# Kernel tuning notes

Hardware: AMD Instinct MI355X
Metric: run time of the kernel (lower is better)

## Reference

```python
import jax, jax.numpy as jnp
import numpy as np

N = 50000          # nodes
E = 800000         # edges (before self-loops)
IN = 128           # in_dim
HID = 128          # hidden_dim
HEADS = 4
G = 256            # graphs in batch
EPS = 1e-5         # batchnorm eps
NEG_SLOPE = 0.2    # GATConv leaky_relu slope


def _gat_layer(x, src, dst, W, a_src, a_dst, bias, H, C, concat):
    """PyG-style GATConv (self-loops already appended to src/dst)."""
    n = x.shape[0]
    h = (x @ W).reshape(n, H, C)                       # [N,H,C]
    s_src = (h * a_src).sum(-1)                        # [N,H]
    s_dst = (h * a_dst).sum(-1)                        # [N,H]
    e = jax.nn.leaky_relu(s_src[src] + s_dst[dst], NEG_SLOPE)   # [E',H]
    m = jax.ops.segment_max(e, dst, num_segments=n)    # segment-wise softmax
    ex = jnp.exp(e - m[dst])
    den = jax.ops.segment_sum(ex, dst, num_segments=n)
    alpha = ex / den[dst]                              # [E',H]
    out = jax.ops.segment_sum(alpha[..., None] * h[src], dst, num_segments=n)  # [N,H,C]
    out = out.reshape(n, H * C) if concat else out.mean(axis=1)
    return out + bias


def _bn(x, gamma, beta):
    # PyG BatchNorm over nodes (training-mode batch statistics)
    mu = x.mean(axis=0)
    var = x.var(axis=0)
    return gamma * (x - mu) * jax.lax.rsqrt(var + EPS) + beta


def setup_inputs() -> dict:
    key = jax.random.key(0)
    ks = jax.random.split(key, 32)
    d = {}
    d["x"] = jax.random.normal(ks[0], (N, IN), dtype=jnp.float32)
    d["edge_index"] = jax.random.randint(ks[1], (2, E), 0, N, dtype=jnp.int64)
    d["batch_idx"] = jnp.sort(jax.random.randint(ks[2], (N,), 0, G, dtype=jnp.int64))
    dims = [(IN, HEADS, HID, True), (HID * HEADS, HEADS, HID, True), (HID * HEADS, 1, HID, False)]
    for i, (din, H, C, concat) in enumerate(dims):
        d[f"W{i}"] = jax.random.normal(ks[3 + 4 * i], (din, H * C), dtype=jnp.float32) * 0.05
        d[f"att_src{i}"] = jax.random.normal(ks[4 + 4 * i], (H, C), dtype=jnp.float32) * 0.05
        d[f"att_dst{i}"] = jax.random.normal(ks[5 + 4 * i], (H, C), dtype=jnp.float32) * 0.05
        out_w = H * C if concat else C
        d[f"bias{i}"] = jnp.zeros((out_w,), dtype=jnp.float32)
        d[f"gamma{i}"] = jnp.ones((out_w,), dtype=jnp.float32)
        d[f"beta{i}"] = jnp.zeros((out_w,), dtype=jnp.float32)
    return d


def reference(x, edge_index, batch_idx,
              W0, att_src0, att_dst0, bias0, gamma0, beta0,
              W1, att_src1, att_dst1, bias1, gamma1, beta1,
              W2, att_src2, att_dst2, bias2, gamma2, beta2):
    n = x.shape[0]
    loops = jnp.arange(n, dtype=edge_index.dtype)
    src = jnp.concatenate([edge_index[0], loops])
    dst = jnp.concatenate([edge_index[1], loops])
    layers = [
        (W0, att_src0, att_dst0, bias0, gamma0, beta0, HEADS, HID, True),
        (W1, att_src1, att_dst1, bias1, gamma1, beta1, HEADS, HID, True),
        (W2, att_src2, att_dst2, bias2, gamma2, beta2, 1, HID, False),
    ]
    h = x
    for (W, a_s, a_d, b, g, bt, H, C, concat) in layers:
        h = _gat_layer(h, src, dst, W, a_s, a_d, b, H, C, concat)
        h = jax.nn.elu(_bn(h, g, bt))
        # dropout: identity in eval mode
    # global_mean_pool over batch_idx
    sums = jax.ops.segment_sum(h, batch_idx, num_segments=G)
    cnt = jax.ops.segment_sum(jnp.ones((n,), dtype=h.dtype), batch_idx, num_segments=G)
    return sums / jnp.maximum(cnt, 1.0)[:, None]
```

## Files before the change

### kernel.cpp

```cpp
#include <hip/hip_runtime.h>
#include <math.h>
#include <stdint.h>

#define N_NODES 50000
#define NPAD    50048
#define N_EDGES 800000
#define EP      (N_EDGES + N_NODES)
#define G_GRAPHS 256
#define BN_EPS   1e-5f
#define NEG_SLOPE 0.2f

typedef float f32x4 __attribute__((ext_vector_type(4)));
typedef _Float16 h16x8 __attribute__((ext_vector_type(8)));

static __device__ __forceinline__ float lrelu(float x) {
    return x > 0.f ? x : NEG_SLOPE * x;
}

static __device__ __forceinline__ void gld_lds16(const void* g, void* l) {
    __builtin_amdgcn_global_load_lds((const __attribute__((address_space(1))) void*)g,
                                     (__attribute__((address_space(3))) void*)l, 16, 0, 0);
}

static __device__ __forceinline__ float2 h2f2(unsigned u) {
    union { unsigned u; _Float16 h[2]; } c;
    c.u = u;
    return make_float2((float)c.h[0], (float)c.h[1]);
}

__global__ void k_hist(const int* __restrict__ ei, int* __restrict__ deg) {
    int stride = gridDim.x * blockDim.x;
    for (int e = blockIdx.x * blockDim.x + threadIdx.x; e < EP; e += stride) {
        int d = (e < N_EDGES) ? ei[N_EDGES + e] : (e - N_EDGES);
        atomicAdd(&deg[d], 1);
    }
}

__global__ void k_scan1(const int* __restrict__ deg, int* __restrict__ row_start,
                        int* __restrict__ totals) {
    __shared__ int buf[1024];
    int t = threadIdx.x;
    int i = blockIdx.x * 1024 + t;
    int v = (i < N_NODES) ? deg[i] : 0;
    buf[t] = v;
    __syncthreads();
    for (int off = 1; off < 1024; off <<= 1) {
        int add = (t >= off) ? buf[t - off] : 0;
        __syncthreads();
        buf[t] += add;
        __syncthreads();
    }
    if (i < N_NODES) row_start[i] = buf[t] - v;
    if (t == 1023) totals[blockIdx.x] = buf[t];
}

__global__ void k_scan2(int* __restrict__ totals, int nb) {
    if (threadIdx.x == 0 && blockIdx.x == 0) {
        int run = 0;
        for (int i = 0; i < nb; ++i) { int v = totals[i]; totals[i] = run; run += v; }
    }
}

__global__ void k_scan3(int* __restrict__ row_start, const int* __restrict__ totals) {
    int i = blockIdx.x * blockDim.x + threadIdx.x;
    if (i < N_NODES) row_start[i] += totals[i >> 10];
    if (i == 0) row_start[N_NODES] = EP;
}

__global__ void k_scatter(const int* __restrict__ ei, const int* __restrict__ row_start,
                          int* __restrict__ cursor, int* __restrict__ csr_src) {
    int stride = gridDim.x * blockDim.x;
    for (int e = blockIdx.x * blockDim.x + threadIdx.x; e < EP; e += stride) {
        int s, d;
        if (e < N_EDGES) { s = ei[e]; d = ei[N_EDGES + e]; }
        else             { s = d = e - N_EDGES; }
        int pos = row_start[d] + atomicAdd(&cursor[d], 1);
        csr_src[pos] = s;
    }
}

__global__ void k_cvtW(const float* __restrict__ W, _Float16* __restrict__ bthi,
                       _Float16* __restrict__ btlo, int Nc, int nsh, int KS) {
    int i = blockIdx.x * 256 + threadIdx.x;
    if (i >= (KS << 5) * Nc) return;
    int k = i >> nsh;
    int n = i & (Nc - 1);
    int c = n >> 7, col = n & 127;
    int ks = k >> 5, kq = (k >> 3) & 3, j = k & 7;
    size_t idx = ((size_t)(c * KS + ks) << 12) + (kq << 10) + (col << 3) + j;
    float v = W[i];
    _Float16 h = (_Float16)v;
    bthi[idx] = h;
    btlo[idx] = (_Float16)(v - (float)h);
}

__global__ void k_bnprep(const float* __restrict__ bnsum, const float* __restrict__ bnsq,
                         const float* __restrict__ gamma, const float* __restrict__ beta,
                         float* __restrict__ scale, float* __restrict__ shift, int W) {
    int f = blockIdx.x * 256 + threadIdx.x;
    if (f >= W) return;
    const float invN = 1.f / (float)N_NODES;
    float mean = bnsum[f] * invN;
    float var  = bnsq[f] * invN - mean * mean;
    float sc = gamma[f] * rsqrtf(var + BN_EPS);
    scale[f] = sc;
    shift[f] = beta[f] - mean * sc;
}

__global__ void k_prepA0(const float* __restrict__ x, _Float16* __restrict__ Aswz,
                         int K, int s8, int KS) {
    int i = blockIdx.x * 256 + threadIdx.x;
    if (i >= NPAD * (K >> 3)) return;
    int r  = i >> s8;
    int c8 = i & ((K >> 3) - 1);
    int k  = c8 << 3;
    union { _Float16 h[8]; uint4 u; } pk;
    if (r < N_NODES) {
        float4 a0 = *(const float4*)&x[(size_t)r * K + k];
        float4 a1 = *(const float4*)&x[(size_t)r * K + k + 4];
        pk.h[0]=(_Float16)a0.x; pk.h[1]=(_Float16)a0.y; pk.h[2]=(_Float16)a0.z; pk.h[3]=(_Float16)a0.w;
        pk.h[4]=(_Float16)a1.x; pk.h[5]=(_Float16)a1.y; pk.h[6]=(_Float16)a1.z; pk.h[7]=(_Float16)a1.w;
    } else {
        pk.u.x = pk.u.y = pk.u.z = pk.u.w = 0u;
    }
    int rb = r >> 7, row = r & 127;
    int ks = k >> 5, kq = (k >> 3) & 3;
    size_t idx = ((size_t)(rb * KS + ks) << 12) + (kq << 10) + (row << 3);
    *(uint4*)&Aswz[idx] = pk.u;
}

__global__ void k_prepA1(const _Float16* __restrict__ act, const float* __restrict__ scale,
                         const float* __restrict__ shift, _Float16* __restrict__ Aswz,
                         int K, int s8, int KS) {
    int i = blockIdx.x * 256 + threadIdx.x;
    if (i >= NPAD * (K >> 3)) return;
    int r  = i >> s8;
    int c8 = i & ((K >> 3) - 1);
    int k  = c8 << 3;
    union { _Float16 h[8]; uint4 u; } pk;
    if (r < N_NODES) {
        uint4 v = *(const uint4*)&act[(size_t)r * K + k];
        float4 sc0 = *(const float4*)&scale[k];
        float4 sc1 = *(const float4*)&scale[k + 4];
        float4 sh0 = *(const float4*)&shift[k];
        float4 sh1 = *(const float4*)&shift[k + 4];
        float2 p0 = h2f2(v.x), p1 = h2f2(v.y), p2 = h2f2(v.z), p3 = h2f2(v.w);
        float y;
        y = fmaf(p0.x, sc0.x, sh0.x); pk.h[0] = (_Float16)(y > 0.f ? y : expm1f(y));
        y = fmaf(p0.y, sc0.y, sh0.y); pk.h[1] = (_Float16)(y > 0.f ? y : expm1f(y));
        y = fmaf(p1.x, sc0.z, sh0.z); pk.h[2] = (_Float16)(y > 0.f ? y : expm1f(y));
        y = fmaf(p1.y, sc0.w, sh0.w); pk.h[3] = (_Float16)(y > 0.f ? y : expm1f(y));
        y = fmaf(p2.x, sc1.x, sh1.x); pk.h[4] = (_Float16)(y > 0.f ? y : expm1f(y));
        y = fmaf(p2.y, sc1.y, sh1.y); pk.h[5] = (_Float16)(y > 0.f ? y : expm1f(y));
        y = fmaf(p3.x, sc1.z, sh1.z); pk.h[6] = (_Float16)(y > 0.f ? y : expm1f(y));
        y = fmaf(p3.y, sc1.w, sh1.w); pk.h[7] = (_Float16)(y > 0.f ? y : expm1f(y));
    } else {
        pk.u.x = pk.u.y = pk.u.z = pk.u.w = 0u;
    }
    int rb = r >> 7, row = r & 127;
    int ks = k >> 5, kq = (k >> 3) & 3;
    size_t idx = ((size_t)(rb * KS + ks) << 12) + (kq << 10) + (row << 3);
    *(uint4*)&Aswz[idx] = pk.u;
}

__launch_bounds__(256)
__global__ void k_gemm_f16(const _Float16* __restrict__ Aswz, const _Float16* __restrict__ bthi,
                           const _Float16* __restrict__ btlo, _Float16* __restrict__ C2,
                           float* __restrict__ sSg, float* __restrict__ sDg,
                           const float* __restrict__ asr, const float* __restrict__ adr,
                           int M, int K, int Nc) {
    __shared__ _Float16 Ah[4096], Bh[4096], Bl[4096];
    __shared__ float rS[128], rD[128];
    const int t    = threadIdx.x;
    const int lane = t & 63, wv = t >> 6;
    const int wr = wv >> 1, wc = wv & 1;
    const int lr = lane & 15, kq = lane >> 4;
    const int r0 = blockIdx.x * 128, c0 = blockIdx.y * 128;
    const int KS = K >> 5;
    const int H = Nc >> 7;
    const int head = blockIdx.y;

    const size_t achunk0 = (size_t)blockIdx.x * KS * 4096;
    const size_t bchunk0 = (size_t)blockIdx.y * KS * 4096;

    f32x4 acc[4][4];
    #pragma unroll
    for (int m = 0; m < 4; ++m)
        #pragma unroll
        for (int n = 0; n < 4; ++n) {
            acc[m][n][0] = 0.f; acc[m][n][1] = 0.f;
            acc[m][n][2] = 0.f; acc[m][n][3] = 0.f;
        }

    for (int ks = 0; ks < KS; ++ks) {
        __syncthreads();
        const _Float16* as  = Aswz + achunk0 + ((size_t)ks << 12);
        const _Float16* bhs = bthi + bchunk0 + ((size_t)ks << 12);
        const _Float16* bls = btlo + bchunk0 + ((size_t)ks << 12);
        #pragma unroll
        for (int p = 0; p < 2; ++p) {
            int ge = p * 2048 + wv * 512 + lane * 8;
            int le = p * 2048 + wv * 512;
            gld_lds16(as  + ge, &Ah[le]);
            gld_lds16(bhs + ge, &Bh[le]);
            gld_lds16(bls + ge, &Bl[le]);
        }
        __syncthreads();

        h16x8 af[4], bfh[4], bfl[4];
        #pragma unroll
        for (int m = 0; m < 4; ++m) {
            int row = wr * 64 + m * 16 + lr;
            af[m] = *(const h16x8*)&Ah[kq * 1024 + row * 8];
        }
        #pragma unroll
        for (int n = 0; n < 4; ++n) {
            int col = wc * 64 + n * 16 + lr;
            bfh[n] = *(const h16x8*)&Bh[kq * 1024 + col * 8];
            bfl[n] = *(const h16x8*)&Bl[kq * 1024 + col * 8];
        }
        #pragma unroll
        for (int m = 0; m < 4; ++m)
            #pragma unroll
            for (int n = 0; n < 4; ++n) {
                acc[m][n] = __builtin_amdgcn_mfma_f32_16x16x32_f16(af[m], bfh[n], acc[m][n], 0, 0, 0);
                acc[m][n] = __builtin_amdgcn_mfma_f32_16x16x32_f16(af[m], bfl[n], acc[m][n], 0, 0, 0);
            }
    }

    float aS[4], aD[4];
    #pragma unroll
    for (int n = 0; n < 4; ++n) {
        int c = c0 + wc * 64 + n * 16 + lr;
        aS[n] = asr[c];
        aD[n] = adr[c];
    }
    __syncthreads();
    if (t < 128) { rS[t] = 0.f; rD[t] = 0.f; }
    __syncthreads();
    #pragma unroll
    for (int m = 0; m < 4; ++m) {
        #pragma unroll
        for (int j = 0; j < 4; ++j) {
            float ps = 0.f, pd = 0.f;
            #pragma unroll
            for (int n = 0; n < 4; ++n) {
                float v = acc[m][n][j];
                ps += v * aS[n];
                pd += v * aD[n];
            }
            #pragma unroll
            for (int off = 1; off < 16; off <<= 1) {
                ps += __shfl_xor(ps, off, 64);
                pd += __shfl_xor(pd, off, 64);
            }
            if (lr == 0) {
                int row = wr * 64 + m * 16 + kq * 4 + j;
                atomicAdd(&rS[row], ps);
                atomicAdd(&rD[row], pd);
            }
        }
    }
    __syncthreads();
    if (t < 128) {
        int r = r0 + t;
        if (r < M) {
            sSg[(size_t)r * H + head] = rS[t];
            sDg[(size_t)r * H + head] = rD[t];
        }
    }

    #pragma unroll
    for (int m = 0; m < 4; ++m) {
        int rowb = r0 + wr * 64 + m * 16 + kq * 4;
        #pragma unroll
        for (int n = 0; n < 4; ++n) {
            int col = c0 + wc * 64 + n * 16 + lr;
            #pragma unroll
            for (int j = 0; j < 4; ++j) {
                int r = rowb + j;
                if (r < M) C2[(size_t)r * Nc + col] = (_Float16)acc[m][n][j];
            }
        }
    }
}

template<int H, int CPT>
__launch_bounds__(256)
__global__ void k_attnagg(const _Float16* __restrict__ hb2, const float* __restrict__ s_src,
                          const float* __restrict__ s_dst, const int* __restrict__ row_start,
                          const int* __restrict__ csr, const float* __restrict__ bias,
                          _Float16* __restrict__ out) {
    const int W = H * 128;
    const int wv = threadIdx.x >> 6;
    const int lane = threadIdx.x & 63;
    const int n = blockIdx.x * 4 + wv;
    if (n >= N_NODES) return;
    const int lo = row_start[n], hi = row_start[n + 1];

    const int h1 = lane & (H - 1);
    const int eo = lane / H;
    const int EPI = 64 / H;
    float sd1 = s_dst[n * H + h1];
    float mx = -INFINITY;
    for (int p = lo + eo; p < hi; p += EPI) {
        float e = lrelu(s_src[csr[p] * H + h1] + sd1);
        mx = fmaxf(mx, e);
    }
    #pragma unroll
    for (int off = H; off < 64; off <<= 1) mx = fmaxf(mx, __shfl_xor(mx, off, 64));
    float sum = 0.f;
    for (int p = lo + eo; p < hi; p += EPI) {
        float e = lrelu(s_src[csr[p] * H + h1] + sd1);
        sum += expf(e - mx);
    }
    #pragma unroll
    for (int off = H; off < 64; off <<= 1) sum += __shfl_xor(sum, off, 64);
    float inv = 1.f / sum;

    const int c0 = lane * CPT;
    const int myh = c0 >> 7;
    float mxv  = __shfl(mx,  myh, 64);
    float invv = __shfl(inv, myh, 64);
    float sdv  = __shfl(sd1, myh, 64);

    float acc[CPT];
    #pragma unroll
    for (int j = 0; j < CPT; ++j) acc[j] = 0.f;

    int p = lo;
    for (; p + 4 <= hi; p += 4) {
        int s0 = csr[p], s1 = csr[p+1], s2 = csr[p+2], s3 = csr[p+3];
        float g0 = s_src[s0 * H + myh], g1 = s_src[s1 * H + myh];
        float g2 = s_src[s2 * H + myh], g3 = s_src[s3 * H + myh];
        if constexpr (CPT == 8) {
            uint4 v0 = *(const uint4*)&hb2[(size_t)s0 * W + c0];
            uint4 v1 = *(const uint4*)&hb2[(size_t)s1 * W + c0];
            uint4 v2 = *(const uint4*)&hb2[(size_t)s2 * W + c0];
            uint4 v3 = *(const uint4*)&hb2[(size_t)s3 * W + c0];
            float a0 = expf(lrelu(g0 + sdv) - mxv) * invv;
            float a1 = expf(lrelu(g1 + sdv) - mxv) * invv;
            float a2 = expf(lrelu(g2 + sdv) - mxv) * invv;
            float a3 = expf(lrelu(g3 + sdv) - mxv) * invv;
            float2 x0, x1, x2, x3;
            x0 = h2f2(v0.x); x1 = h2f2(v0.y); x2 = h2f2(v0.z); x3 = h2f2(v0.w);
            acc[0] += a0*x0.x; acc[1] += a0*x0.y; acc[2] += a0*x1.x; acc[3] += a0*x1.y;
            acc[4] += a0*x2.x; acc[5] += a0*x2.y; acc[6] += a0*x3.x; acc[7] += a0*x3.y;
            x0 = h2f2(v1.x); x1 = h2f2(v1.y); x2 = h2f2(v1.z); x3 = h2f2(v1.w);
            acc[0] += a1*x0.x; acc[1] += a1*x0.y; acc[2] += a1*x1.x; acc[3] += a1*x1.y;
            acc[4] += a1*x2.x; acc[5] += a1*x2.y; acc[6] += a1*x3.x; acc[7] += a1*x3.y;
            x0 = h2f2(v2.x); x1 = h2f2(v2.y); x2 = h2f2(v2.z); x3 = h2f2(v2.w);
            acc[0] += a2*x0.x; acc[1] += a2*x0.y; acc[2] += a2*x1.x; acc[3] += a2*x1.y;
            acc[4] += a2*x2.x; acc[5] += a2*x2.y; acc[6] += a2*x3.x; acc[7] += a2*x3.y;
            x0 = h2f2(v3.x); x1 = h2f2(v3.y); x2 = h2f2(v3.z); x3 = h2f2(v3.w);
            acc[0] += a3*x0.x; acc[1] += a3*x0.y; acc[2] += a3*x1.x; acc[3] += a3*x1.y;
            acc[4] += a3*x2.x; acc[5] += a3*x2.y; acc[6] += a3*x3.x; acc[7] += a3*x3.y;
        } else {
            unsigned v0 = *(const unsigned*)&hb2[(size_t)s0 * W + c0];
            unsigned v1 = *(const unsigned*)&hb2[(size_t)s1 * W + c0];
            unsigned v2 = *(const unsigned*)&hb2[(size_t)s2 * W + c0];
            unsigned v3 = *(const unsigned*)&hb2[(size_t)s3 * W + c0];
            float a0 = expf(lrelu(g0 + sdv) - mxv) * invv;
            float a1 = expf(lrelu(g1 + sdv) - mxv) * invv;
            float a2 = expf(lrelu(g2 + sdv) - mxv) * invv;
            float a3 = expf(lrelu(g3 + sdv) - mxv) * invv;
            float2 x;
            x = h2f2(v0); acc[0] += a0*x.x; acc[1] += a0*x.y;
            x = h2f2(v1); acc[0] += a1*x.x; acc[1] += a1*x.y;
            x = h2f2(v2); acc[0] += a2*x.x; acc[1] += a2*x.y;
            x = h2f2(v3); acc[0] += a3*x.x; acc[1] += a3*x.y;
        }
    }
    for (; p < hi; ++p) {
        int s0 = csr[p];
        float a0 = expf(lrelu(s_src[s0 * H + myh] + sdv) - mxv) * invv;
        if constexpr (CPT == 8) {
            uint4 v0 = *(const uint4*)&hb2[(size_t)s0 * W + c0];
            float2 x0 = h2f2(v0.x), x1 = h2f2(v0.y), x2 = h2f2(v0.z), x3 = h2f2(v0.w);
            acc[0] += a0*x0.x; acc[1] += a0*x0.y; acc[2] += a0*x1.x; acc[3] += a0*x1.y;
            acc[4] += a0*x2.x; acc[5] += a0*x2.y; acc[6] += a0*x3.x; acc[7] += a0*x3.y;
        } else {
            float2 x = h2f2(*(const unsigned*)&hb2[(size_t)s0 * W + c0]);
            acc[0] += a0*x.x; acc[1] += a0*x.y;
        }
    }

    union { _Float16 h[CPT]; uint4 u4; unsigned u1; } pk;
    #pragma unroll
    for (int j = 0; j < CPT; ++j) pk.h[j] = (_Float16)(acc[j] + bias[c0 + j]);
    if constexpr (CPT == 8)
        *(uint4*)&out[(size_t)n * W + c0] = pk.u4;
    else
        *(unsigned*)&out[(size_t)n * W + c0] = pk.u1;
}

__global__ void k_bnstat2(const _Float16* __restrict__ x, float* __restrict__ bnsum,
                          float* __restrict__ bnsq, int W) {
    const int RPB = 64;
    int t  = threadIdx.x;
    int r0 = blockIdx.x * RPB;
    int r1 = min(r0 + RPB, N_NODES);
    float s0 = 0.f, q0 = 0.f, s1 = 0.f, q1 = 0.f;
    for (int r = r0; r < r1; ++r) {
        float2 v = h2f2(*(const unsigned*)&x[(size_t)r * W + 2 * t]);
        s0 += v.x; q0 += v.x * v.x;
        s1 += v.y; q1 += v.y * v.y;
    }
    atomicAdd(&bnsum[2*t],   s0);
    atomicAdd(&bnsq[2*t],    q0);
    atomicAdd(&bnsum[2*t+1], s1);
    atomicAdd(&bnsq[2*t+1],  q1);
}

__global__ void k_pool(const _Float16* __restrict__ x, const int* __restrict__ batch,
                       const float* __restrict__ scale, const float* __restrict__ shift,
                       float* __restrict__ out) {
    int g = blockIdx.x;
    int f = threadIdx.x;
    int a = 0, b = N_NODES;
    while (a < b) { int m = (a + b) >> 1; if (batch[m] < g) a = m + 1; else b = m; }
    int lo = a;
    b = N_NODES;
    while (a < b) { int m = (a + b) >> 1; if (batch[m] < g + 1) a = m + 1; else b = m; }
    int hi = a;
    float sc = scale[f], sh = shift[f];
    float s = 0.f;
    for (int r = lo; r < hi; ++r) {
        float v = (float)x[(size_t)r * 128 + f];
        float y = fmaf(v, sc, sh);
        s += (y > 0.f) ? y : expm1f(y);
    }
    int cnt = hi - lo;
    out[g * 128 + f] = s / (float)(cnt > 0 ? cnt : 1);
}

extern "C" void kernel_launch(void* const* d_in, const int* in_sizes, int n_in,
                              void* d_out, int out_size, void* d_ws, size_t ws_size,
                              hipStream_t stream) {
    const float* x     = (const float*)d_in[0];
    const int*   ei    = (const int*)d_in[1];
    const int*   batch = (const int*)d_in[2];
    const float* Wm[3]  = {(const float*)d_in[3],  (const float*)d_in[9],  (const float*)d_in[15]};
    const float* asr[3] = {(const float*)d_in[4],  (const float*)d_in[10], (const float*)d_in[16]};
    const float* adr[3] = {(const float*)d_in[5],  (const float*)d_in[11], (const float*)d_in[17]};
    const float* bia[3] = {(const float*)d_in[6],  (const float*)d_in[12], (const float*)d_in[18]};
    const float* gam[3] = {(const float*)d_in[7],  (const float*)d_in[13], (const float*)d_in[19]};
    const float* bet[3] = {(const float*)d_in[8],  (const float*)d_in[14], (const float*)d_in[20]};

    char* w = (char*)d_ws;
    auto alloc = [&](size_t bytes) -> void* {
        void* p = (void*)w;
        w += (bytes + 255) & ~(size_t)255;
        return p;
    };
    _Float16* act2   = (_Float16*)alloc((size_t)N_NODES * 512 * 2);
    _Float16* act128 = (_Float16*)alloc((size_t)N_NODES * 128 * 2);
    _Float16* hb2    = (_Float16*)alloc((size_t)N_NODES * 512 * 2);
    _Float16* Aswz   = (_Float16*)alloc((size_t)NPAD * 512 * 2);
    int* csr_src   = (int*)alloc((size_t)EP * 4);
    int* row_start = (int*)alloc((size_t)(N_NODES + 1) * 4);
    int* deg       = (int*)alloc((size_t)N_NODES * 4);
    int* cursor    = (int*)alloc((size_t)N_NODES * 4);
    float* s_src = (float*)alloc((size_t)N_NODES * 4 * 4);
    float* s_dst = (float*)alloc((size_t)N_NODES * 4 * 4);
    float* bn    = (float*)alloc(1024 * 4);
    float* scl   = (float*)alloc(512 * 4);
    float* shf   = (float*)alloc(512 * 4);
    int* totals  = (int*)alloc(64 * 4);
    _Float16* bthi = (_Float16*)alloc((size_t)512 * 512 * 2);
    _Float16* btlo = (_Float16*)alloc((size_t)512 * 512 * 2);

    hipMemsetAsync(deg, 0, (size_t)N_NODES * 4, stream);
    hipMemsetAsync(cursor, 0, (size_t)N_NODES * 4, stream);
    k_hist<<<512, 256, 0, stream>>>(ei, deg);
    k_scan1<<<(N_NODES + 1023) / 1024, 1024, 0, stream>>>(deg, row_start, totals);
    k_scan2<<<1, 64, 0, stream>>>(totals, (N_NODES + 1023) / 1024);
    k_scan3<<<(N_NODES + 255) / 256, 256, 0, stream>>>(row_start, totals);
    k_scatter<<<512, 256, 0, stream>>>(ei, row_start, cursor, csr_src);

    auto layer = [&](int K, int li, int H, bool first, _Float16* outAct) {
        int Wd = H * 128;
        int nsh = (Wd == 512) ? 9 : 7;
        int KS = K >> 5;
        int s8 = (K == 512) ? 6 : 4;
        int tot = K * Wd;
        k_cvtW<<<(tot + 255) / 256, 256, 0, stream>>>(Wm[li], bthi, btlo, Wd, nsh, KS);
        int ptot = NPAD * (K >> 3);
        if (first)
            k_prepA0<<<(ptot + 255) / 256, 256, 0, stream>>>(x, Aswz, K, s8, KS);
        else
            k_prepA1<<<(ptot + 255) / 256, 256, 0, stream>>>(act2, scl, shf, Aswz, K, s8, KS);
        dim3 gg(NPAD / 128, Wd / 128);
        k_gemm_f16<<<gg, 256, 0, stream>>>(Aswz, bthi, btlo, hb2, s_src, s_dst,
                                           asr[li], adr[li], N_NODES, K, Wd);
        int nb = (N_NODES + 3) / 4;
        if (H == 4)
            k_attnagg<4, 8><<<nb, 256, 0, stream>>>(hb2, s_src, s_dst, row_start, csr_src,
                                                    bia[li], outAct);
        else
            k_attnagg<1, 2><<<nb, 256, 0, stream>>>(hb2, s_src, s_dst, row_start, csr_src,
                                                    bia[li], outAct);
        hipMemsetAsync(bn, 0, 1024 * 4, stream);
        k_bnstat2<<<(N_NODES + 63) / 64, Wd / 2, 0, stream>>>(outAct, bn, bn + 512, Wd);
        k_bnprep<<<(Wd + 255) / 256, 256, 0, stream>>>(bn, bn + 512, gam[li], bet[li], scl, shf, Wd);
    };

    layer(128, 0, 4, true,  act2);
    layer(512, 1, 4, false, act2);
    layer(512, 2, 1, false, act128);

    k_pool<<<G_GRAPHS, 128, 0, stream>>>(act128, batch, scl, shf, (float*)d_out);
}
```

Measured before the change: 902.5 us.

## Drop fp16 weight residual split and cache attention logits in LDS

The GEMM no longer carries a low-order fp16 residual of the weights, which halves the B-tile loads and the MFMA count. The cost is weight precision, now a single fp16 rounding. The aggregation kernel gains a fast path for nodes with degree up to 256: it computes the edge logits and exponentials once into per-wave LDS and reuses them, instead of recomputing exp and re-gathering s_src during feature accumulation. The softmax normalisation is folded into the final write. The gather loop is widened to 8 edges, and the high-degree fallback now does one edge per iteration.

```diff
diff --git a/kernel.cpp b/kernel.cpp
--- a/kernel.cpp
+++ b/kernel.cpp
@@ -80,7 +80,7 @@
 }
 
 __global__ void k_cvtW(const float* __restrict__ W, _Float16* __restrict__ bthi,
-                       _Float16* __restrict__ btlo, int Nc, int nsh, int KS) {
+                       int Nc, int nsh, int KS) {
     int i = blockIdx.x * 256 + threadIdx.x;
     if (i >= (KS << 5) * Nc) return;
     int k = i >> nsh;
@@ -88,10 +88,7 @@
     int c = n >> 7, col = n & 127;
     int ks = k >> 5, kq = (k >> 3) & 3, j = k & 7;
     size_t idx = ((size_t)(c * KS + ks) << 12) + (kq << 10) + (col << 3) + j;
-    float v = W[i];
-    _Float16 h = (_Float16)v;
-    bthi[idx] = h;
-    btlo[idx] = (_Float16)(v - (float)h);
+    bthi[idx] = (_Float16)W[i];
 }
 
 __global__ void k_bnprep(const float* __restrict__ bnsum, const float* __restrict__ bnsq,
@@ -165,11 +162,11 @@
 
 __launch_bounds__(256)
 __global__ void k_gemm_f16(const _Float16* __restrict__ Aswz, const _Float16* __restrict__ bthi,
-                           const _Float16* __restrict__ btlo, _Float16* __restrict__ C2,
+                           _Float16* __restrict__ C2,
                            float* __restrict__ sSg, float* __restrict__ sDg,
                            const float* __restrict__ asr, const float* __restrict__ adr,
                            int M, int K, int Nc) {
-    __shared__ _Float16 Ah[4096], Bh[4096], Bl[4096];
+    __shared__ _Float16 Ah[4096], Bh[4096];
     __shared__ float rS[128], rD[128];
     const int t    = threadIdx.x;
     const int lane = t & 63, wv = t >> 6;
@@ -196,18 +193,16 @@
         __syncthreads();
         const _Float16* as  = Aswz + achunk0 + ((size_t)ks << 12);
         const _Float16* bhs = bthi + bchunk0 + ((size_t)ks << 12);
-        const _Float16* bls = btlo + bchunk0 + ((size_t)ks << 12);
         #pragma unroll
         for (int p = 0; p < 2; ++p) {
             int ge = p * 2048 + wv * 512 + lane * 8;
             int le = p * 2048 + wv * 512;
             gld_lds16(as  + ge, &Ah[le]);
             gld_lds16(bhs + ge, &Bh[le]);
-            gld_lds16(bls + ge, &Bl[le]);
         }
         __syncthreads();
 
-        h16x8 af[4], bfh[4], bfl[4];
+        h16x8 af[4], bfh[4];
         #pragma unroll
         for (int m = 0; m < 4; ++m) {
             int row = wr * 64 + m * 16 + lr;
@@ -217,15 +212,12 @@
         for (int n = 0; n < 4; ++n) {
             int col = wc * 64 + n * 16 + lr;
             bfh[n] = *(const h16x8*)&Bh[kq * 1024 + col * 8];
-            bfl[n] = *(const h16x8*)&Bl[kq * 1024 + col * 8];
         }
         #pragma unroll
         for (int m = 0; m < 4; ++m)
             #pragma unroll
-            for (int n = 0; n < 4; ++n) {
+            for (int n = 0; n < 4; ++n)
                 acc[m][n] = __builtin_amdgcn_mfma_f32_16x16x32_f16(af[m], bfh[n], acc[m][n], 0, 0, 0);
-                acc[m][n] = __builtin_amdgcn_mfma_f32_16x16x32_f16(af[m], bfl[n], acc[m][n], 0, 0, 0);
-            }
     }
 
     float aS[4], aD[4];
@@ -285,23 +277,107 @@
     }
 }
 
-template<int H, int CPT>
+template<int H, int CPT, int CAP>
 __launch_bounds__(256)
 __global__ void k_attnagg(const _Float16* __restrict__ hb2, const float* __restrict__ s_src,
                           const float* __restrict__ s_dst, const int* __restrict__ row_start,
                           const int* __restrict__ csr, const float* __restrict__ bias,
                           _Float16* __restrict__ out) {
     const int W = H * 128;
+    __shared__ float alds[4][CAP * H];
     const int wv = threadIdx.x >> 6;
     const int lane = threadIdx.x & 63;
     const int n = blockIdx.x * 4 + wv;
     if (n >= N_NODES) return;
     const int lo = row_start[n], hi = row_start[n + 1];
+    const int deg = hi - lo;
 
     const int h1 = lane & (H - 1);
     const int eo = lane / H;
     const int EPI = 64 / H;
     float sd1 = s_dst[n * H + h1];
+    const int c0 = lane * CPT;
+    const int myh = c0 >> 7;
+
+    float acc[CPT];
+    #pragma unroll
+    for (int j = 0; j < CPT; ++j) acc[j] = 0.f;
+
+    if (deg <= CAP) {
+        float* al = &alds[wv][0];
+        float mx = -INFINITY;
+        for (int q = eo; q < deg; q += EPI) {
+            float e = lrelu(s_src[csr[lo + q] * H + h1] + sd1);
+            al[q * H + h1] = e;
+            mx = fmaxf(mx, e);
+        }
+        #pragma unroll
+        for (int off = H; off < 64; off <<= 1) mx = fmaxf(mx, __shfl_xor(mx, off, 64));
+        float sum = 0.f;
+        for (int q = eo; q < deg; q += EPI) {
+            float ex = expf(al[q * H + h1] - mx);
+            al[q * H + h1] = ex;
+            sum += ex;
+        }
+        #pragma unroll
+        for (int off = H; off < 64; off <<= 1) sum += __shfl_xor(sum, off, 64);
+        float invv = __shfl(1.f / sum, myh, 64);
+        asm volatile("s_waitcnt lgkmcnt(0)" ::: "memory");
+        __builtin_amdgcn_sched_barrier(0);
+
+        int q = 0;
+        for (; q + 8 <= deg; q += 8) {
+            int s[8];
+            #pragma unroll
+            for (int j = 0; j < 8; ++j) s[j] = csr[lo + q + j];
+            float a[8];
+            #pragma unroll
+            for (int j = 0; j < 8; ++j) a[j] = al[(q + j) * H + myh];
+            if constexpr (CPT == 8) {
+                uint4 v[8];
+                #pragma unroll
+                for (int j = 0; j < 8; ++j) v[j] = *(const uint4*)&hb2[(size_t)s[j] * W + c0];
+                #pragma unroll
+                for (int j = 0; j < 8; ++j) {
+                    float2 x0 = h2f2(v[j].x), x1 = h2f2(v[j].y), x2 = h2f2(v[j].z), x3 = h2f2(v[j].w);
+                    acc[0] += a[j]*x0.x; acc[1] += a[j]*x0.y; acc[2] += a[j]*x1.x; acc[3] += a[j]*x1.y;
+                    acc[4] += a[j]*x2.x; acc[5] += a[j]*x2.y; acc[6] += a[j]*x3.x; acc[7] += a[j]*x3.y;
+                }
+            } else {
+                unsigned v[8];
+                #pragma unroll
+                for (int j = 0; j < 8; ++j) v[j] = *(const unsigned*)&hb2[(size_t)s[j] * W + c0];
+                #pragma unroll
+                for (int j = 0; j < 8; ++j) {
+                    float2 x = h2f2(v[j]);
+                    acc[0] += a[j]*x.x; acc[1] += a[j]*x.y;
+                }
+            }
+        }
+        for (; q < deg; ++q) {
+            int s0 = csr[lo + q];
+            float a0 = al[q * H + myh];
+            if constexpr (CPT == 8) {
+                uint4 v0 = *(const uint4*)&hb2[(size_t)s0 * W + c0];
+                float2 x0 = h2f2(v0.x), x1 = h2f2(v0.y), x2 = h2f2(v0.z), x3 = h2f2(v0.w);
+                acc[0] += a0*x0.x; acc[1] += a0*x0.y; acc[2] += a0*x1.x; acc[3] += a0*x1.y;
+                acc[4] += a0*x2.x; acc[5] += a0*x2.y; acc[6] += a0*x3.x; acc[7] += a0*x3.y;
+            } else {
+                float2 x = h2f2(*(const unsigned*)&hb2[(size_t)s0 * W + c0]);
+                acc[0] += a0*x.x; acc[1] += a0*x.y;
+            }
+        }
+
+        union { _Float16 h[CPT]; uint4 u4; unsigned u1; } pk;
+        #pragma unroll
+        for (int j = 0; j < CPT; ++j) pk.h[j] = (_Float16)(fmaf(acc[j], invv, bias[c0 + j]));
+        if constexpr (CPT == 8)
+            *(uint4*)&out[(size_t)n * W + c0] = pk.u4;
+        else
+            *(unsigned*)&out[(size_t)n * W + c0] = pk.u1;
+        return;
+    }
+
     float mx = -INFINITY;
     for (int p = lo + eo; p < hi; p += EPI) {
         float e = lrelu(s_src[csr[p] * H + h1] + sd1);
@@ -318,62 +394,13 @@
     for (int off = H; off < 64; off <<= 1) sum += __shfl_xor(sum, off, 64);
     float inv = 1.f / sum;
 
-    const int c0 = lane * CPT;
-    const int myh = c0 >> 7;
     float mxv  = __shfl(mx,  myh, 64);
     float invv = __shfl(inv, myh, 64);
     float sdv  = __shfl(sd1, myh, 64);
 
-    float acc[CPT];
-    #pragma unroll
-    for (int j = 0; j < CPT; ++j) acc[j] = 0.f;
-
-    int p = lo;
-    for (; p + 4 <= hi; p += 4) {
-        int s0 = csr[p], s1 = csr[p+1], s2 = csr[p+2], s3 = csr[p+3];
-        float g0 = s_src[s0 * H + myh], g1 = s_src[s1 * H + myh];
-        float g2 = s_src[s2 * H + myh], g3 = s_src[s3 * H + myh];
-        if constexpr (CPT == 8) {
-            uint4 v0 = *(const uint4*)&hb2[(size_t)s0 * W + c0];
-            uint4 v1 = *(const uint4*)&hb2[(size_t)s1 * W + c0];
-            uint4 v2 = *(const uint4*)&hb2[(size_t)s2 * W + c0];
-            uint4 v3 = *(const uint4*)&hb2[(size_t)s3 * W + c0];
-            float a0 = expf(lrelu(g0 + sdv) - mxv) * invv;
-            float a1 = expf(lrelu(g1 + sdv) - mxv) * invv;
-            float a2 = expf(lrelu(g2 + sdv) - mxv) * invv;
-            float a3 = expf(lrelu(g3 + sdv) - mxv) * invv;
-            float2 x0, x1, x2, x3;
-            x0 = h2f2(v0.x); x1 = h2f2(v0.y); x2 = h2f2(v0.z); x3 = h2f2(v0.w);
-            acc[0] += a0*x0.x; acc[1] += a0*x0.y; acc[2] += a0*x1.x; acc[3] += a0*x1.y;
-            acc[4] += a0*x2.x; acc[5] += a0*x2.y; acc[6] += a0*x3.x; acc[7] += a0*x3.y;
-            x0 = h2f2(v1.x); x1 = h2f2(v1.y); x2 = h2f2(v1.z); x3 = h2f2(v1.w);
-            acc[0] += a1*x0.x; acc[1] += a1*x0.y; acc[2] += a1*x1.x; acc[3] += a1*x1.y;
-            acc[4] += a1*x2.x; acc[5] += a1*x2.y; acc[6] += a1*x3.x; acc[7] += a1*x3.y;
-            x0 = h2f2(v2.x); x1 = h2f2(v2.y); x2 = h2f2(v2.z); x3 = h2f2(v2.w);
-            acc[0] += a2*x0.x; acc[1] += a2*x0.y; acc[2] += a2*x1.x; acc[3] += a2*x1.y;
-            acc[4] += a2*x2.x; acc[5] += a2*x2.y; acc[6] += a2*x3.x; acc[7] += a2*x3.y;
-            x0 = h2f2(v3.x); x1 = h2f2(v3.y); x2 = h2f2(v3.z); x3 = h2f2(v3.w);
-            acc[0] += a3*x0.x; acc[1] += a3*x0.y; acc[2] += a3*x1.x; acc[3] += a3*x1.y;
-            acc[4] += a3*x2.x; acc[5] += a3*x2.y; acc[6] += a3*x3.x; acc[7] += a3*x3.y;
-        } else {
-            unsigned v0 = *(const unsigned*)&hb2[(size_t)s0 * W + c0];
-            unsigned v1 = *(const unsigned*)&hb2[(size_t)s1 * W + c0];
-            unsigned v2 = *(const unsigned*)&hb2[(size_t)s2 * W + c0];
-            unsigned v3 = *(const unsigned*)&hb2[(size_t)s3 * W + c0];
-            float a0 = expf(lrelu(g0 + sdv) - mxv) * invv;
-            float a1 = expf(lrelu(g1 + sdv) - mxv) * invv;
-            float a2 = expf(lrelu(g2 + sdv) - mxv) * invv;
-            float a3 = expf(lrelu(g3 + sdv) - mxv) * invv;
-            float2 x;
-            x = h2f2(v0); acc[0] += a0*x.x; acc[1] += a0*x.y;
-            x = h2f2(v1); acc[0] += a1*x.x; acc[1] += a1*x.y;
-            x = h2f2(v2); acc[0] += a2*x.x; acc[1] += a2*x.y;
-            x = h2f2(v3); acc[0] += a3*x.x; acc[1] += a3*x.y;
-        }
-    }
-    for (; p < hi; ++p) {
+    for (int p = lo; p < hi; ++p) {
         int s0 = csr[p];
-        float a0 = expf(lrelu(s_src[s0 * H + myh] + sdv) - mxv) * invv;
+        float a0 = expf(lrelu(s_src[s0 * H + myh] + sdv) - mxv);
         if constexpr (CPT == 8) {
             uint4 v0 = *(const uint4*)&hb2[(size_t)s0 * W + c0];
             float2 x0 = h2f2(v0.x), x1 = h2f2(v0.y), x2 = h2f2(v0.z), x3 = h2f2(v0.w);
@@ -384,10 +411,9 @@
             acc[0] += a0*x.x; acc[1] += a0*x.y;
         }
     }
-
     union { _Float16 h[CPT]; uint4 u4; unsigned u1; } pk;
     #pragma unroll
-    for (int j = 0; j < CPT; ++j) pk.h[j] = (_Float16)(acc[j] + bias[c0 + j]);
+    for (int j = 0; j < CPT; ++j) pk.h[j] = (_Float16)(fmaf(acc[j], invv, bias[c0 + j]));
     if constexpr (CPT == 8)
         *(uint4*)&out[(size_t)n * W + c0] = pk.u4;
     else
@@ -468,7 +494,6 @@
     float* shf   = (float*)alloc(512 * 4);
     int* totals  = (int*)alloc(64 * 4);
     _Float16* bthi = (_Float16*)alloc((size_t)512 * 512 * 2);
-    _Float16* btlo = (_Float16*)alloc((size_t)512 * 512 * 2);
 
     hipMemsetAsync(deg, 0, (size_t)N_NODES * 4, stream);
     hipMemsetAsync(cursor, 0, (size_t)N_NODES * 4, stream);
@@ -484,22 +509,22 @@
         int KS = K >> 5;
         int s8 = (K == 512) ? 6 : 4;
         int tot = K * Wd;
-        k_cvtW<<<(tot + 255) / 256, 256, 0, stream>>>(Wm[li], bthi, btlo, Wd, nsh, KS);
+        k_cvtW<<<(tot + 255) / 256, 256, 0, stream>>>(Wm[li], bthi, Wd, nsh, KS);
         int ptot = NPAD * (K >> 3);
         if (first)
             k_prepA0<<<(ptot + 255) / 256, 256, 0, stream>>>(x, Aswz, K, s8, KS);
         else
             k_prepA1<<<(ptot + 255) / 256, 256, 0, stream>>>(act2, scl, shf, Aswz, K, s8, KS);
         dim3 gg(NPAD / 128, Wd / 128);
-        k_gemm_f16<<<gg, 256, 0, stream>>>(Aswz, bthi, btlo, hb2, s_src, s_dst,
+        k_gemm_f16<<<gg, 256, 0, stream>>>(Aswz, bthi, hb2, s_src, s_dst,
                                            asr[li], adr[li], N_NODES, K, Wd);
         int nb = (N_NODES + 3) / 4;
         if (H == 4)
-            k_attnagg<4, 8><<<nb, 256, 0, stream>>>(hb2, s_src, s_dst, row_start, csr_src,
-                                                    bia[li], outAct);
+            k_attnagg<4, 8, 256><<<nb, 256, 0, stream>>>(hb2, s_src, s_dst, row_start, csr_src,
+                                                         bia[li], outAct);
         else
-            k_attnagg<1, 2><<<nb, 256, 0, stream>>>(hb2, s_src, s_dst, row_start, csr_src,
-                                                    bia[li], outAct);
+            k_attnagg<1, 2, 256><<<nb, 256, 0, stream>>>(hb2, s_src, s_dst, row_start, csr_src,
+                                                         bia[li], outAct);
         hipMemsetAsync(bn, 0, 1024 * 4, stream);
         k_bnstat2<<<(N_NODES + 63) / 64, Wd / 2, 0, stream>>>(outAct, bn, bn + 512, Wd);
         k_bnprep<<<(Wd + 255) / 256, 256, 0, stream>>>(bn, bn + 512, gam[li], bet[li], scl, shf, Wd);
```

New measurement: 853.4 us. 1.06x faster.
